# Kernel optimization log

Hardware: AMD Instinct MI355X
Metric: run time of the kernel (lower is better)

## Reference

```python
import jax, jax.numpy as jnp
import numpy as np

B = 1024      # total windows (batch*windows_per_image)
W = 7         # window_size
T = W * W     # tokens per window = 49
C = 256       # scaled_emb_dim = emb_dim * 2**level
H = 8         # heads
D = C // H    # head_dim = 32
NUM_POS = 2 * W - 1


def _relative_pos():
    coords = np.arange(W)
    coords = np.stack(np.meshgrid(coords, coords, indexing='ij')).reshape(2, -1)
    rp = coords[:, :, None] - coords[:, None, :] + (W - 1)
    return jnp.asarray(rp, dtype=jnp.int32)  # (2, T, T)


def setup_inputs() -> dict:
    key = jax.random.key(0)
    ks = jax.random.split(key, 12)
    s = 0.02
    return {
        'x': jax.random.normal(ks[0], (B, T, C), dtype=jnp.float32),
        'relative_pos': _relative_pos(),
        'bias_table': jax.random.truncated_normal(ks[1], -2.0, 2.0, (H, NUM_POS, NUM_POS), dtype=jnp.float32) * s,
        'wq': jax.random.normal(ks[2], (C, H, D), dtype=jnp.float32) / np.sqrt(C),
        'bq': jnp.zeros((H, D), dtype=jnp.float32),
        'wk': jax.random.normal(ks[3], (C, H, D), dtype=jnp.float32) / np.sqrt(C),
        'bk': jnp.zeros((H, D), dtype=jnp.float32),
        'wv': jax.random.normal(ks[4], (C, H, D), dtype=jnp.float32) / np.sqrt(C),
        'bv': jnp.zeros((H, D), dtype=jnp.float32),
        'wo': jax.random.normal(ks[5], (H, D, C), dtype=jnp.float32) / np.sqrt(C),
        'bo': jnp.zeros((C,), dtype=jnp.float32),
        'dw': jax.random.normal(ks[6], (C, C), dtype=jnp.float32) / np.sqrt(C),
        'db': jnp.zeros((C,), dtype=jnp.float32),
    }


def reference(x, relative_pos, bias_table, wq, bq, wk, bk, wv, bv, wo, bo, dw, db):
    # QKV projections (flax DenseGeneral with bias)
    q = jnp.einsum('btc,chd->bthd', x, wq) + bq  # (B,T,H,D)
    k = jnp.einsum('btc,chd->bthd', x, wk) + bk
    v = jnp.einsum('btc,chd->bthd', x, wv) + bv

    # gathered relative position bias: (H, T, T)
    bias = bias_table[:, relative_pos[0], relative_pos[1]]

    # attention logits with query scaling (flax dot_product_attention)
    q = q / jnp.sqrt(jnp.asarray(D, dtype=q.dtype))
    logits = jnp.einsum('bqhd,bkhd->bhqk', q, k) + bias[None]
    attn = jax.nn.softmax(logits, axis=-1)

    out = jnp.einsum('bhqk,bkhd->bqhd', attn, v)
    y = jnp.einsum('bqhd,hdc->bqc', out, wo) + bo  # attention out projection
    y = jnp.einsum('btc,cf->btf', y, dw) + db      # trailing Dense(scaled_emb_dim)
    return y
```

## Files before the change

kernel.cpp:

```cpp
#include <hip/hip_runtime.h>
#include <stdint.h>

#define T 49
#define CCH 256

typedef __bf16 bf16x8 __attribute__((ext_vector_type(8)));
typedef float f32x4 __attribute__((ext_vector_type(4)));

static __device__ __forceinline__ unsigned short f2bf(float f){
  uint32_t u = __builtin_bit_cast(uint32_t, f);
  u = u + 0x7fffu + ((u >> 16) & 1u);
  return (unsigned short)(u >> 16);
}
static __device__ __forceinline__ float bf2f(unsigned short h){
  return __builtin_bit_cast(float, ((uint32_t)h) << 16);
}
static __device__ __forceinline__ uint32_t pk2(float a, float b){
  return (uint32_t)f2bf(a) | ((uint32_t)f2bf(b) << 16);
}
static __device__ __forceinline__ f32x4 mfma16(bf16x8 a, bf16x8 b, f32x4 c){
  return __builtin_amdgcn_mfma_f32_16x16x32_bf16(a, b, c, 0, 0, 0);
}
#define SWZ(row) ((((row) & 7) << 4))

static __device__ __forceinline__ bf16x8 build_frag(uint32_t lo_w0, uint32_t lo_w1,
                                                    uint32_t hi_w0, uint32_t hi_w1,
                                                    int srcA, int srcB, bool use_hi){
  uint32_t a0 = (uint32_t)__shfl((int)lo_w0, srcA, 64);
  uint32_t c0 = (uint32_t)__shfl((int)hi_w0, srcA, 64);
  uint32_t a1 = (uint32_t)__shfl((int)lo_w1, srcA, 64);
  uint32_t c1 = (uint32_t)__shfl((int)hi_w1, srcA, 64);
  uint32_t a2 = (uint32_t)__shfl((int)lo_w0, srcB, 64);
  uint32_t c2 = (uint32_t)__shfl((int)hi_w0, srcB, 64);
  uint32_t a3 = (uint32_t)__shfl((int)lo_w1, srcB, 64);
  uint32_t c3 = (uint32_t)__shfl((int)hi_w1, srcB, 64);
  uint4 u = use_hi ? make_uint4(c0, c1, c2, c3) : make_uint4(a0, a1, a2, a3);
  return __builtin_bit_cast(bf16x8, u);
}


__global__ void prep_wqkvT(const float* __restrict__ wq, const float* __restrict__ wk,
                           const float* __restrict__ wv, unsigned short* __restrict__ out){
  int bk = blockIdx.x;
  int p = bk >> 8, kk = bk & 255;
  int n = threadIdx.x;
  const float* w = (p == 0) ? wq : (p == 1 ? wk : wv);
  float scl = (p == 0) ? 0.17677669529663687f : 1.0f;
  out[(size_t)(p * 256 + n) * 256 + kk] = f2bf(w[kk * 256 + n] * scl);
}

__global__ void prep_wodT(const float* __restrict__ wo, const float* __restrict__ dw,
                          unsigned short* __restrict__ out){
  int hd = blockIdx.x;
  int c = threadIdx.x;
  float s = 0.f;
  for (int cp = 0; cp < 256; ++cp) s = fmaf(wo[hd * 256 + cp], dw[cp * 256 + c], s);
  out[(size_t)c * 256 + hd] = f2bf(s);
}

__global__ void prep_misc(const int* __restrict__ rp, const float* __restrict__ btab,
                          const float* __restrict__ bq, const float* __restrict__ bk,
                          const float* __restrict__ bv, const float* __restrict__ bo,
                          const float* __restrict__ dwm, const float* __restrict__ db,
                          unsigned short* __restrict__ biasP, float* __restrict__ bqkv,
                          float* __restrict__ bod){
  int t = threadIdx.x;
  if (blockIdx.x == 0){
    for (int idx = t; idx < 768; idx += 256){
      int p = idx >> 8, n = idx & 255;
      float v = (p == 0) ? bq[n] * 0.17677669529663687f : (p == 1 ? bk[n] : bv[n]);
      bqkv[idx] = v;
    }
    float s = db[t];
    for (int cp = 0; cp < 256; ++cp) s = fmaf(bo[cp], dwm[cp * 256 + t], s);
    bod[t] = s;
  } else {
    int h = blockIdx.x - 1;
    for (int idx = t; idx < 4096; idx += 256){
      int r  = idx & 3;
      int lo = (idx >> 2) & 15;
      int g  = (idx >> 6) & 3;
      int nt = (idx >> 8) & 3;
      int jt = idx >> 10;
      int j = 16 * jt + 4 * g + r;
      int i = 16 * nt + lo;
      float v;
      if (j >= T) v = -1e30f;
      else if (i >= T) v = 0.f;
      else {
        int r0 = rp[i * 49 + j];
        int r1 = rp[2401 + i * 49 + j];
        v = btab[h * 169 + r0 * 13 + r1];
      }
      biasP[h * 4096 + idx] = f2bf(v);
    }
  }
}

__launch_bounds__(512, 4)
__global__ void wmsa_main(const float* __restrict__ x,
                          const unsigned short* __restrict__ wqkvT,
                          const unsigned short* __restrict__ wodT,
                          const unsigned short* __restrict__ biasP,
                          const float* __restrict__ bqkv,
                          const float* __restrict__ bod,
                          float* __restrict__ y){
  __shared__ unsigned short xs[64 * 256];

  const int b    = blockIdx.x;
  const int tid  = threadIdx.x;
  const int h    = tid >> 6;
  const int lane = tid & 63;
  const int g    = lane >> 4;
  const int lo   = lane & 15;
  char* xs_c = (char*)xs;

  const float* xb = x + (size_t)b * T * CCH;
  for (int idx = tid; idx < 64 * 64; idx += 512){
    int row = idx >> 6, c4 = idx & 63;
    float4 v = make_float4(0.f, 0.f, 0.f, 0.f);
    if (row < T) v = reinterpret_cast<const float4*>(xb)[row * 64 + c4];
    *reinterpret_cast<uint2*>(xs_c + row * 512 + ((c4 * 8) ^ SWZ(row)))
        = make_uint2(pk2(v.x, v.y), pk2(v.z, v.w));
  }
  __syncthreads();

  const int  srcA = lo + 16 * ((2 * g) & 3);
  const int  srcB = lo + 16 * ((2 * g + 1) & 3);
  const bool ghi  = (g >= 2);

  bf16x8 av[2][2];
  {
    f32x4 avc[4][2];
    #pragma unroll
    for (int mt = 0; mt < 4; ++mt)
      #pragma unroll
      for (int nt = 0; nt < 2; ++nt) avc[mt][nt] = f32x4{0,0,0,0};

    #pragma unroll 1
    for (int kt = 0; kt < 8; ++kt){
      bf16x8 ax[4];
      #pragma unroll
      for (int mt = 0; mt < 4; ++mt){
        int row = 16 * mt + lo;
        ax[mt] = *reinterpret_cast<const bf16x8*>(xs_c + row * 512 + ((kt * 64 + 16 * g) ^ SWZ(row)));
      }
      #pragma unroll
      for (int nt = 0; nt < 2; ++nt){
        const bf16x8 wvf = *reinterpret_cast<const bf16x8*>(
            wqkvT + (size_t)(512 + h * 32 + 16 * nt + lo) * 256 + kt * 32 + 8 * g);
        #pragma unroll
        for (int mt = 0; mt < 4; ++mt) avc[mt][nt] = mfma16(ax[mt], wvf, avc[mt][nt]);
      }
    }
    uint32_t pv[4][2][2];
    #pragma unroll
    for (int nt = 0; nt < 2; ++nt){
      const float bvs = bqkv[512 + h * 32 + 16 * nt + lo];
      #pragma unroll
      for (int mt = 0; mt < 4; ++mt){
        f32x4 tv = avc[mt][nt];
        tv[0] += bvs; tv[1] += bvs; tv[2] += bvs; tv[3] += bvs;
        pv[mt][nt][0] = pk2(tv[0], tv[1]); pv[mt][nt][1] = pk2(tv[2], tv[3]);
      }
    }
    #pragma unroll
    for (int dt = 0; dt < 2; ++dt)
      #pragma unroll
      for (int ktj = 0; ktj < 2; ++ktj)
        av[dt][ktj] = build_frag(pv[2 * ktj][dt][0], pv[2 * ktj][dt][1],
                                 pv[2 * ktj + 1][dt][0], pv[2 * ktj + 1][dt][1], srcA, srcB, ghi);
  }

  bf16x8 fk[4];
  {
    f32x4 akk[2][4];
    #pragma unroll
    for (int mt = 0; mt < 2; ++mt)
      #pragma unroll
      for (int nt = 0; nt < 4; ++nt) akk[mt][nt] = f32x4{0,0,0,0};

    #pragma unroll 1
    for (int kt = 0; kt < 8; ++kt){
      bf16x8 bx[4];
      #pragma unroll
      for (int nt = 0; nt < 4; ++nt){
        int row = 16 * nt + lo;
        bx[nt] = *reinterpret_cast<const bf16x8*>(xs_c + row * 512 + ((kt * 64 + 16 * g) ^ SWZ(row)));
      }
      #pragma unroll
      for (int mt = 0; mt < 2; ++mt){
        const bf16x8 wkf = *reinterpret_cast<const bf16x8*>(
            wqkvT + (size_t)(256 + h * 32 + 16 * mt + lo) * 256 + kt * 32 + 8 * g);
        #pragma unroll
        for (int nt = 0; nt < 4; ++nt) akk[mt][nt] = mfma16(wkf, bx[nt], akk[mt][nt]);
      }
    }
    uint32_t pkk[2][4][2];
    #pragma unroll
    for (int mt = 0; mt < 2; ++mt){
      const float4 b4k = *reinterpret_cast<const float4*>(bqkv + 256 + h * 32 + 16 * mt + 4 * g);
      #pragma unroll
      for (int nt = 0; nt < 4; ++nt){
        f32x4 tk = akk[mt][nt];
        tk[0] += b4k.x; tk[1] += b4k.y; tk[2] += b4k.z; tk[3] += b4k.w;
        pkk[mt][nt][0] = pk2(tk[0], tk[1]); pkk[mt][nt][1] = pk2(tk[2], tk[3]);
      }
    }
    #pragma unroll
    for (int nt = 0; nt < 4; ++nt)
      fk[nt] = build_frag(pkk[0][nt][0], pkk[0][nt][1], pkk[1][nt][0], pkk[1][nt][1], srcA, srcB, ghi);
  }

  bf16x8 fq[4];
  {
    f32x4 aq[2][4];
    #pragma unroll
    for (int mt = 0; mt < 2; ++mt)
      #pragma unroll
      for (int nt = 0; nt < 4; ++nt) aq[mt][nt] = f32x4{0,0,0,0};

    #pragma unroll 1
    for (int kt = 0; kt < 8; ++kt){
      bf16x8 bx[4];
      #pragma unroll
      for (int nt = 0; nt < 4; ++nt){
        int row = 16 * nt + lo;
        bx[nt] = *reinterpret_cast<const bf16x8*>(xs_c + row * 512 + ((kt * 64 + 16 * g) ^ SWZ(row)));
      }
      #pragma unroll
      for (int mt = 0; mt < 2; ++mt){
        const bf16x8 wqf = *reinterpret_cast<const bf16x8*>(
            wqkvT + (size_t)(h * 32 + 16 * mt + lo) * 256 + kt * 32 + 8 * g);
        #pragma unroll
        for (int nt = 0; nt < 4; ++nt) aq[mt][nt] = mfma16(wqf, bx[nt], aq[mt][nt]);
      }
    }
    uint32_t pq[2][4][2];
    #pragma unroll
    for (int mt = 0; mt < 2; ++mt){
      const float4 b4q = *reinterpret_cast<const float4*>(bqkv + h * 32 + 16 * mt + 4 * g);
      #pragma unroll
      for (int nt = 0; nt < 4; ++nt){
        f32x4 tq = aq[mt][nt];
        tq[0] += b4q.x; tq[1] += b4q.y; tq[2] += b4q.z; tq[3] += b4q.w;
        pq[mt][nt][0] = pk2(tq[0], tq[1]); pq[mt][nt][1] = pk2(tq[2], tq[3]);
      }
    }
    #pragma unroll
    for (int nt = 0; nt < 4; ++nt)
      fq[nt] = build_frag(pq[0][nt][0], pq[0][nt][1], pq[1][nt][0], pq[1][nt][1], srcA, srcB, ghi);
  }
  __syncthreads();

  #pragma unroll 1
  for (int nt = 0; nt < 4; ++nt){
    f32x4 lacc[4];
    #pragma unroll
    for (int jt = 0; jt < 4; ++jt){
      lacc[jt] = mfma16(fk[jt], fq[nt], f32x4{0,0,0,0});
      const uint2 bb = *reinterpret_cast<const uint2*>(
          biasP + h * 4096 + jt * 1024 + nt * 256 + (g * 16 + lo) * 4);
      lacc[jt][0] += bf2f((unsigned short)(bb.x & 0xffff));
      lacc[jt][1] += bf2f((unsigned short)(bb.x >> 16));
      lacc[jt][2] += bf2f((unsigned short)(bb.y & 0xffff));
      lacc[jt][3] += bf2f((unsigned short)(bb.y >> 16));
    }
    float m = -3.0e38f;
    #pragma unroll
    for (int jt = 0; jt < 4; ++jt)
      #pragma unroll
      for (int r = 0; r < 4; ++r) m = fmaxf(m, lacc[jt][r]);
    m = fmaxf(m, __shfl_xor(m, 16, 64));
    m = fmaxf(m, __shfl_xor(m, 32, 64));
    float ssum = 0.f;
    uint32_t pw[4][2];
    #pragma unroll
    for (int jt = 0; jt < 4; ++jt){
      f32x4 t = lacc[jt];
      #pragma unroll
      for (int r = 0; r < 4; ++r){
        t[r] = exp2f((t[r] - m) * 1.4426950408889634f);
        ssum += t[r];
      }
      pw[jt][0] = pk2(t[0], t[1]);
      pw[jt][1] = pk2(t[2], t[3]);
    }
    ssum += __shfl_xor(ssum, 16, 64);
    ssum += __shfl_xor(ssum, 32, 64);
    const float r0 = 1.f / ssum;

    bf16x8 pf0 = build_frag(pw[0][0], pw[0][1], pw[1][0], pw[1][1], srcA, srcB, ghi);
    bf16x8 pf1 = build_frag(pw[2][0], pw[2][1], pw[3][0], pw[3][1], srcA, srcB, ghi);

    const int i = 16 * nt + lo;
    #pragma unroll
    for (int dt = 0; dt < 2; ++dt){
      f32x4 oacc = mfma16(av[dt][0], pf0, f32x4{0,0,0,0});
      oacc = mfma16(av[dt][1], pf1, oacc);
      *reinterpret_cast<uint2*>(xs_c + i * 512 + ((h * 64 + dt * 32 + g * 8) ^ SWZ(i)))
          = make_uint2(pk2(oacc[0] * r0, oacc[1] * r0), pk2(oacc[2] * r0, oacc[3] * r0));
    }
  }
  __syncthreads();

  f32x4 facc[4][2];
  #pragma unroll
  for (int mt = 0; mt < 4; ++mt)
    #pragma unroll
    for (int nt = 0; nt < 2; ++nt) facc[mt][nt] = f32x4{0,0,0,0};

  #pragma unroll 1
  for (int kt = 0; kt < 8; ++kt){
    bf16x8 a[4];
    #pragma unroll
    for (int mt = 0; mt < 4; ++mt){
      int row = 16 * mt + lo;
      a[mt] = *reinterpret_cast<const bf16x8*>(xs_c + row * 512 + ((kt * 64 + 16 * g) ^ SWZ(row)));
    }
    #pragma unroll
    for (int nt = 0; nt < 2; ++nt){
      int crow = h * 32 + nt * 16 + lo;
      const bf16x8 bfr = *reinterpret_cast<const bf16x8*>(wodT + (size_t)crow * 256 + kt * 32 + 8 * g);
      #pragma unroll
      for (int mt = 0; mt < 4; ++mt) facc[mt][nt] = mfma16(a[mt], bfr, facc[mt][nt]);
    }
  }
  #pragma unroll
  for (int nt = 0; nt < 2; ++nt){
    int c = h * 32 + nt * 16 + lo;
    float bd = bod[c];
    #pragma unroll
    for (int mt = 0; mt < 4; ++mt)
      #pragma unroll
      for (int r = 0; r < 4; ++r){
        int i = 16 * mt + 4 * g + r;
        if (i < T) y[((size_t)b * T + i) * CCH + c] = facc[mt][nt][r] + bd;
      }
  }
}

extern "C" void kernel_launch(void* const* d_in, const int* in_sizes, int n_in,
                              void* d_out, int out_size, void* d_ws, size_t ws_size,
                              hipStream_t stream){
  const float* x    = (const float*)d_in[0];
  const int*   rp   = (const int*)d_in[1];
  const float* btab = (const float*)d_in[2];
  const float* wq   = (const float*)d_in[3];
  const float* bq   = (const float*)d_in[4];
  const float* wk   = (const float*)d_in[5];
  const float* bk   = (const float*)d_in[6];
  const float* wv   = (const float*)d_in[7];
  const float* bv   = (const float*)d_in[8];
  const float* wo   = (const float*)d_in[9];
  const float* bo   = (const float*)d_in[10];
  const float* dw   = (const float*)d_in[11];
  const float* db   = (const float*)d_in[12];
  float* y = (float*)d_out;

  char* ws = (char*)d_ws;
  unsigned short* wqkvT = (unsigned short*)(ws);
  unsigned short* wodT  = (unsigned short*)(ws + 393216);
  unsigned short* biasP = (unsigned short*)(ws + 524288);
  float* bqkv           = (float*)(ws + 589824);
  float* bod            = (float*)(ws + 592896);

  prep_wqkvT<<<768, 256, 0, stream>>>(wq, wk, wv, wqkvT);
  prep_wodT<<<256, 256, 0, stream>>>(wo, dw, wodT);
  prep_misc<<<9, 256, 0, stream>>>(rp, btab, bq, bk, bv, bo, dw, db, biasP, bqkv, bod);
  wmsa_main<<<1024, 512, 0, stream>>>(x, wqkvT, wodT, biasP, bqkv, bod, y);
}
```

Before: 144.0 us.

## Batch weight loads, stage V through LDS, prefetch bias and x loads

Groups the global weight-fragment loads for the Q, K, V and output projections into blocks of 2 or 4 k-steps issued ahead of the MFMAs, so more memory requests are in flight. V is now written transposed into a new LDS buffer and read back during PV instead of being held in registers via shuffles. The relative-position bias loads are hoisted ahead of the logits MFMAs, x loads are issued all at once before conversion, and the bf16 conversion uses the native cast. These add LDS usage (an extra 32KB) and register pressure, which may reduce occupancy.

```diff
diff --git a/kernel.cpp b/kernel.cpp
--- a/kernel.cpp
+++ b/kernel.cpp
@@ -8,9 +8,8 @@
 typedef float f32x4 __attribute__((ext_vector_type(4)));
 
 static __device__ __forceinline__ unsigned short f2bf(float f){
-  uint32_t u = __builtin_bit_cast(uint32_t, f);
-  u = u + 0x7fffu + ((u >> 16) & 1u);
-  return (unsigned short)(u >> 16);
+  __bf16 h = (__bf16)f;
+  return __builtin_bit_cast(unsigned short, h);
 }
 static __device__ __forceinline__ float bf2f(unsigned short h){
   return __builtin_bit_cast(float, ((uint32_t)h) << 16);
@@ -106,6 +105,7 @@
                           const float* __restrict__ bod,
                           float* __restrict__ y){
   __shared__ unsigned short xs[64 * 256];
+  __shared__ unsigned short vts[8 * 32 * 64];
 
   const int b    = blockIdx.x;
   const int tid  = threadIdx.x;
@@ -116,12 +116,22 @@
   char* xs_c = (char*)xs;
 
   const float* xb = x + (size_t)b * T * CCH;
-  for (int idx = tid; idx < 64 * 64; idx += 512){
-    int row = idx >> 6, c4 = idx & 63;
-    float4 v = make_float4(0.f, 0.f, 0.f, 0.f);
-    if (row < T) v = reinterpret_cast<const float4*>(xb)[row * 64 + c4];
-    *reinterpret_cast<uint2*>(xs_c + row * 512 + ((c4 * 8) ^ SWZ(row)))
-        = make_uint2(pk2(v.x, v.y), pk2(v.z, v.w));
+  {
+    float4 vv[8];
+    #pragma unroll
+    for (int k2 = 0; k2 < 8; ++k2){
+      int idx = tid + k2 * 512;
+      int row = idx >> 6, c4 = idx & 63;
+      vv[k2] = make_float4(0.f, 0.f, 0.f, 0.f);
+      if (row < T) vv[k2] = reinterpret_cast<const float4*>(xb)[row * 64 + c4];
+    }
+    #pragma unroll
+    for (int k2 = 0; k2 < 8; ++k2){
+      int idx = tid + k2 * 512;
+      int row = idx >> 6, c4 = idx & 63;
+      *reinterpret_cast<uint2*>(xs_c + row * 512 + ((c4 * 8) ^ SWZ(row)))
+          = make_uint2(pk2(vv[k2].x, vv[k2].y), pk2(vv[k2].z, vv[k2].w));
+    }
   }
   __syncthreads();
 
@@ -129,7 +139,6 @@
   const int  srcB = lo + 16 * ((2 * g + 1) & 3);
   const bool ghi  = (g >= 2);
 
-  bf16x8 av[2][2];
   {
     f32x4 avc[4][2];
     #pragma unroll
@@ -138,38 +147,40 @@
       for (int nt = 0; nt < 2; ++nt) avc[mt][nt] = f32x4{0,0,0,0};
 
     #pragma unroll 1
-    for (int kt = 0; kt < 8; ++kt){
-      bf16x8 ax[4];
-      #pragma unroll
-      for (int mt = 0; mt < 4; ++mt){
-        int row = 16 * mt + lo;
-        ax[mt] = *reinterpret_cast<const bf16x8*>(xs_c + row * 512 + ((kt * 64 + 16 * g) ^ SWZ(row)));
-      }
-      #pragma unroll
-      for (int nt = 0; nt < 2; ++nt){
-        const bf16x8 wvf = *reinterpret_cast<const bf16x8*>(
-            wqkvT + (size_t)(512 + h * 32 + 16 * nt + lo) * 256 + kt * 32 + 8 * g);
-        #pragma unroll
-        for (int mt = 0; mt < 4; ++mt) avc[mt][nt] = mfma16(ax[mt], wvf, avc[mt][nt]);
-      }
-    }
-    uint32_t pv[4][2][2];
+    for (int kb = 0; kb < 2; ++kb){
+      bf16x8 wv[2][4];
+      #pragma unroll
+      for (int nt = 0; nt < 2; ++nt)
+        #pragma unroll
+        for (int q4 = 0; q4 < 4; ++q4)
+          wv[nt][q4] = *reinterpret_cast<const bf16x8*>(
+              wqkvT + (size_t)(512 + h * 32 + 16 * nt + lo) * 256 + (kb * 4 + q4) * 32 + 8 * g);
+      #pragma unroll
+      for (int q4 = 0; q4 < 4; ++q4){
+        int kt = kb * 4 + q4;
+        bf16x8 ax[4];
+        #pragma unroll
+        for (int mt = 0; mt < 4; ++mt){
+          int row = 16 * mt + lo;
+          ax[mt] = *reinterpret_cast<const bf16x8*>(xs_c + row * 512 + ((kt * 64 + 16 * g) ^ SWZ(row)));
+        }
+        #pragma unroll
+        for (int nt = 0; nt < 2; ++nt)
+          #pragma unroll
+          for (int mt = 0; mt < 4; ++mt) avc[mt][nt] = mfma16(ax[mt], wv[nt][q4], avc[mt][nt]);
+      }
+    }
     #pragma unroll
     for (int nt = 0; nt < 2; ++nt){
       const float bvs = bqkv[512 + h * 32 + 16 * nt + lo];
+      const int d = 16 * nt + lo;
       #pragma unroll
       for (int mt = 0; mt < 4; ++mt){
-        f32x4 tv = avc[mt][nt];
-        tv[0] += bvs; tv[1] += bvs; tv[2] += bvs; tv[3] += bvs;
-        pv[mt][nt][0] = pk2(tv[0], tv[1]); pv[mt][nt][1] = pk2(tv[2], tv[3]);
-      }
-    }
-    #pragma unroll
-    for (int dt = 0; dt < 2; ++dt)
-      #pragma unroll
-      for (int ktj = 0; ktj < 2; ++ktj)
-        av[dt][ktj] = build_frag(pv[2 * ktj][dt][0], pv[2 * ktj][dt][1],
-                                 pv[2 * ktj + 1][dt][0], pv[2 * ktj + 1][dt][1], srcA, srcB, ghi);
+        f32x4 t = avc[mt][nt];
+        *reinterpret_cast<uint2*>((char*)vts + h * 4096 + d * 128 + ((mt * 32 + g * 8) ^ SWZ(d)))
+            = make_uint2(pk2(t[0] + bvs, t[1] + bvs), pk2(t[2] + bvs, t[3] + bvs));
+      }
+    }
   }
 
   bf16x8 fk[4];
@@ -181,19 +192,27 @@
       for (int nt = 0; nt < 4; ++nt) akk[mt][nt] = f32x4{0,0,0,0};
 
     #pragma unroll 1
-    for (int kt = 0; kt < 8; ++kt){
-      bf16x8 bx[4];
-      #pragma unroll
-      for (int nt = 0; nt < 4; ++nt){
-        int row = 16 * nt + lo;
-        bx[nt] = *reinterpret_cast<const bf16x8*>(xs_c + row * 512 + ((kt * 64 + 16 * g) ^ SWZ(row)));
-      }
-      #pragma unroll
-      for (int mt = 0; mt < 2; ++mt){
-        const bf16x8 wkf = *reinterpret_cast<const bf16x8*>(
-            wqkvT + (size_t)(256 + h * 32 + 16 * mt + lo) * 256 + kt * 32 + 8 * g);
-        #pragma unroll
-        for (int nt = 0; nt < 4; ++nt) akk[mt][nt] = mfma16(wkf, bx[nt], akk[mt][nt]);
+    for (int kb = 0; kb < 2; ++kb){
+      bf16x8 wk[2][4];
+      #pragma unroll
+      for (int mt = 0; mt < 2; ++mt)
+        #pragma unroll
+        for (int q4 = 0; q4 < 4; ++q4)
+          wk[mt][q4] = *reinterpret_cast<const bf16x8*>(
+              wqkvT + (size_t)(256 + h * 32 + 16 * mt + lo) * 256 + (kb * 4 + q4) * 32 + 8 * g);
+      #pragma unroll
+      for (int q4 = 0; q4 < 4; ++q4){
+        int kt = kb * 4 + q4;
+        bf16x8 bx[4];
+        #pragma unroll
+        for (int nt = 0; nt < 4; ++nt){
+          int row = 16 * nt + lo;
+          bx[nt] = *reinterpret_cast<const bf16x8*>(xs_c + row * 512 + ((kt * 64 + 16 * g) ^ SWZ(row)));
+        }
+        #pragma unroll
+        for (int mt = 0; mt < 2; ++mt)
+          #pragma unroll
+          for (int nt = 0; nt < 4; ++nt) akk[mt][nt] = mfma16(wk[mt][q4], bx[nt], akk[mt][nt]);
       }
     }
     uint32_t pkk[2][4][2];
@@ -221,19 +240,27 @@
       for (int nt = 0; nt < 4; ++nt) aq[mt][nt] = f32x4{0,0,0,0};
 
     #pragma unroll 1
-    for (int kt = 0; kt < 8; ++kt){
-      bf16x8 bx[4];
-      #pragma unroll
-      for (int nt = 0; nt < 4; ++nt){
-        int row = 16 * nt + lo;
-        bx[nt] = *reinterpret_cast<const bf16x8*>(xs_c + row * 512 + ((kt * 64 + 16 * g) ^ SWZ(row)));
-      }
-      #pragma unroll
-      for (int mt = 0; mt < 2; ++mt){
-        const bf16x8 wqf = *reinterpret_cast<const bf16x8*>(
-            wqkvT + (size_t)(h * 32 + 16 * mt + lo) * 256 + kt * 32 + 8 * g);
-        #pragma unroll
-        for (int nt = 0; nt < 4; ++nt) aq[mt][nt] = mfma16(wqf, bx[nt], aq[mt][nt]);
+    for (int kb = 0; kb < 4; ++kb){
+      bf16x8 wq2[2][2];
+      #pragma unroll
+      for (int mt = 0; mt < 2; ++mt)
+        #pragma unroll
+        for (int q2 = 0; q2 < 2; ++q2)
+          wq2[mt][q2] = *reinterpret_cast<const bf16x8*>(
+              wqkvT + (size_t)(h * 32 + 16 * mt + lo) * 256 + (kb * 2 + q2) * 32 + 8 * g);
+      #pragma unroll
+      for (int q2 = 0; q2 < 2; ++q2){
+        int kt = kb * 2 + q2;
+        bf16x8 bx[4];
+        #pragma unroll
+        for (int nt = 0; nt < 4; ++nt){
+          int row = 16 * nt + lo;
+          bx[nt] = *reinterpret_cast<const bf16x8*>(xs_c + row * 512 + ((kt * 64 + 16 * g) ^ SWZ(row)));
+        }
+        #pragma unroll
+        for (int mt = 0; mt < 2; ++mt)
+          #pragma unroll
+          for (int nt = 0; nt < 4; ++nt) aq[mt][nt] = mfma16(wq2[mt][q2], bx[nt], aq[mt][nt]);
       }
     }
     uint32_t pq[2][4][2];
@@ -253,18 +280,22 @@
   }
   __syncthreads();
 
+  const char* vb = (const char*)vts + h * 4096;
   #pragma unroll 1
   for (int nt = 0; nt < 4; ++nt){
+    uint2 bb[4];
+    #pragma unroll
+    for (int jt = 0; jt < 4; ++jt)
+      bb[jt] = *reinterpret_cast<const uint2*>(
+          biasP + h * 4096 + jt * 1024 + nt * 256 + (g * 16 + lo) * 4);
     f32x4 lacc[4];
     #pragma unroll
     for (int jt = 0; jt < 4; ++jt){
       lacc[jt] = mfma16(fk[jt], fq[nt], f32x4{0,0,0,0});
-      const uint2 bb = *reinterpret_cast<const uint2*>(
-          biasP + h * 4096 + jt * 1024 + nt * 256 + (g * 16 + lo) * 4);
-      lacc[jt][0] += bf2f((unsigned short)(bb.x & 0xffff));
-      lacc[jt][1] += bf2f((unsigned short)(bb.x >> 16));
-      lacc[jt][2] += bf2f((unsigned short)(bb.y & 0xffff));
-      lacc[jt][3] += bf2f((unsigned short)(bb.y >> 16));
+      lacc[jt][0] += bf2f((unsigned short)(bb[jt].x & 0xffff));
+      lacc[jt][1] += bf2f((unsigned short)(bb[jt].x >> 16));
+      lacc[jt][2] += bf2f((unsigned short)(bb[jt].y & 0xffff));
+      lacc[jt][3] += bf2f((unsigned short)(bb[jt].y >> 16));
     }
     float m = -3.0e38f;
     #pragma unroll
@@ -296,8 +327,11 @@
     const int i = 16 * nt + lo;
     #pragma unroll
     for (int dt = 0; dt < 2; ++dt){
-      f32x4 oacc = mfma16(av[dt][0], pf0, f32x4{0,0,0,0});
-      oacc = mfma16(av[dt][1], pf1, oacc);
+      int row = 16 * dt + lo;
+      bf16x8 av0 = *reinterpret_cast<const bf16x8*>(vb + row * 128 + ((16 * g) ^ SWZ(row)));
+      bf16x8 av1 = *reinterpret_cast<const bf16x8*>(vb + row * 128 + ((64 + 16 * g) ^ SWZ(row)));
+      f32x4 oacc = mfma16(av0, pf0, f32x4{0,0,0,0});
+      oacc = mfma16(av1, pf1, oacc);
       *reinterpret_cast<uint2*>(xs_c + i * 512 + ((h * 64 + dt * 32 + g * 8) ^ SWZ(i)))
           = make_uint2(pk2(oacc[0] * r0, oacc[1] * r0), pk2(oacc[2] * r0, oacc[3] * r0));
     }
@@ -311,19 +345,27 @@
     for (int nt = 0; nt < 2; ++nt) facc[mt][nt] = f32x4{0,0,0,0};
 
   #pragma unroll 1
-  for (int kt = 0; kt < 8; ++kt){
-    bf16x8 a[4];
-    #pragma unroll
-    for (int mt = 0; mt < 4; ++mt){
-      int row = 16 * mt + lo;
-      a[mt] = *reinterpret_cast<const bf16x8*>(xs_c + row * 512 + ((kt * 64 + 16 * g) ^ SWZ(row)));
-    }
-    #pragma unroll
-    for (int nt = 0; nt < 2; ++nt){
-      int crow = h * 32 + nt * 16 + lo;
-      const bf16x8 bfr = *reinterpret_cast<const bf16x8*>(wodT + (size_t)crow * 256 + kt * 32 + 8 * g);
-      #pragma unroll
-      for (int mt = 0; mt < 4; ++mt) facc[mt][nt] = mfma16(a[mt], bfr, facc[mt][nt]);
+  for (int kb = 0; kb < 2; ++kb){
+    bf16x8 wod[2][4];
+    #pragma unroll
+    for (int nt = 0; nt < 2; ++nt)
+      #pragma unroll
+      for (int q4 = 0; q4 < 4; ++q4)
+        wod[nt][q4] = *reinterpret_cast<const bf16x8*>(
+            wodT + (size_t)(h * 32 + nt * 16 + lo) * 256 + (kb * 4 + q4) * 32 + 8 * g);
+    #pragma unroll
+    for (int q4 = 0; q4 < 4; ++q4){
+      int kt = kb * 4 + q4;
+      bf16x8 a[4];
+      #pragma unroll
+      for (int mt = 0; mt < 4; ++mt){
+        int row = 16 * mt + lo;
+        a[mt] = *reinterpret_cast<const bf16x8*>(xs_c + row * 512 + ((kt * 64 + 16 * g) ^ SWZ(row)));
+      }
+      #pragma unroll
+      for (int nt = 0; nt < 2; ++nt)
+        #pragma unroll
+        for (int mt = 0; mt < 4; ++mt) facc[mt][nt] = mfma16(a[mt], wod[nt][q4], facc[mt][nt]);
     }
   }
   #pragma unroll
```

Result: faster. 134.2 us (-6.8%).
